# Kernel optimization log

Measured on AMD Instinct MI355X. Metric: run time of the kernel, lower is better.

Reference implementation:

```python
import jax, jax.numpy as jnp
import numpy as np

# Video-DiT scale: d_model = H * D = 2048
B, S_T, S_C, H, D = 2, 2048, 1024, 16, 128


def setup_inputs() -> dict:
    key = jax.random.key(0)
    ks = jax.random.split(key, 6)
    f = lambda k, s: jax.random.normal(k, s, dtype=jnp.float32)
    return {
        "target_q": f(ks[0], (B, S_T, H, D)),
        "target_k": f(ks[1], (B, S_T, H, D)),
        "target_v": f(ks[2], (B, S_T, H, D)),
        "cond_k": f(ks[3], (B, S_C, H, D)),
        "cond_v": f(ks[4], (B, S_C, H, D)),
        "b_param": f(ks[5], (1,)),
    }


def reference(target_q, target_k, target_v, cond_k, cond_v, b_param):
    """Extended target self-attention over [target_k; cond_k] with a scalar
    logit bias b_param added only to the condition-key columns.
    Inputs BSHD; returns [B, S_t, H*D] (ready for output_proj)."""
    Bq, St, Hh, Dd = target_q.shape
    Sc = cond_k.shape[1]
    scale = Dd ** -0.5  # softmax_scale defaults to head_dim**-0.5

    k_ext = jnp.concatenate([target_k, cond_k], axis=1)  # [B, S_t+S_c, H, D]
    v_ext = jnp.concatenate([target_v, cond_v], axis=1)

    # [B, H, S_t, S_t+S_c]
    logits = jnp.einsum('bqhd,bkhd->bhqk', target_q, k_ext) * jnp.asarray(scale, target_q.dtype)
    # bias: 0 on target keys, b on cond keys
    bias = jnp.concatenate([
        jnp.zeros((St,), logits.dtype),
        jnp.broadcast_to(b_param.astype(logits.dtype), (Sc,)),
    ])
    logits = logits + bias[None, None, None, :]

    probs = jax.nn.softmax(logits, axis=-1)
    out = jnp.einsum('bhqk,bkhd->bqhd', probs, v_ext)  # [B, S_t, H, D]
    return out.reshape(Bq, St, Hh * Dd)
```

## Files before the change

kernel.cpp:

```cpp
#include <hip/hip_runtime.h>
#include <hip/hip_bf16.h>

typedef __attribute__((ext_vector_type(4))) float f32x4;
typedef __attribute__((ext_vector_type(16))) float f32x16;
typedef __attribute__((ext_vector_type(8))) short bf8;
typedef __attribute__((ext_vector_type(2))) int i32x2;

#define B_ 2
#define ST 2048
#define SC 1024
#define SK 3072
#define NH 16
#define DH 128
#define KVB 32
#define NT 96
#define TGT 64
#define SCALE 0.088388347648318447f
#define LOG2E 1.4426950408889634f
#define PRE_TILE_U32 2048
#define PRE_BYTES (32ull * 96 * 512 * 16)
#define WS_NEED (2ull * PRE_BYTES)

__device__ __forceinline__ i32x2 tr_read(unsigned a) {
    i32x2 d;
    asm volatile("ds_read_b64_tr_b16 %0, %1" : "=v"(d) : "v"(a));
    return d;
}

__device__ __forceinline__ unsigned cvtpk(float lo, float hi) {
    unsigned r;
    asm("v_cvt_pk_bf16_f32 %0, %1, %2" : "=v"(r) : "v"(lo), "v"(hi));
    return r;
}

__device__ __forceinline__ void swap32(unsigned &a, unsigned &b) {
    asm volatile("v_permlane32_swap_b32 %0, %1" : "+v"(a), "+v"(b));
}

__device__ __forceinline__ bf8 mk_bf8(i32x2 a, i32x2 b) {
    union { i32x2 h[2]; bf8 v; } u;
    u.h[0] = a; u.h[1] = b;
    return u.v;
}
__device__ __forceinline__ bf8 mk_bf8w(unsigned w0, unsigned w1, unsigned w2, unsigned w3) {
    union { unsigned w[4]; bf8 v; } u;
    u.w[0] = w0; u.w[1] = w1; u.w[2] = w2; u.w[3] = w3;
    return u.v;
}
__device__ __forceinline__ bf8 pack_bf8(f32x4 a, f32x4 b) {
    return mk_bf8w(cvtpk(a[0], a[1]), cvtpk(a[2], a[3]),
                   cvtpk(b[0], b[1]), cvtpk(b[2], b[3]));
}

__global__ __launch_bounds__(256)
void preconv(const float* __restrict__ TK, const float* __restrict__ TV,
             const float* __restrict__ CK, const float* __restrict__ CV,
             unsigned* __restrict__ KP, unsigned* __restrict__ VP)
{
    const unsigned gid = blockIdx.x * 256 + threadIdx.x;
    const int c    = gid & 511;
    const int idx  = gid >> 9;
    const int bhid = idx / 96;
    const int t    = idx - bhid * 96;
    const int bb   = bhid >> 4;
    const int hh   = bhid & 15;

    const int krow = c >> 4;
    const int kcol = ((c & 15) ^ (krow & 7)) << 3;
    const int gkv  = t * 32 + krow;
    const float* kp = (gkv < ST)
        ? TK + (((size_t)bb * ST + gkv) * NH + hh) * DH + kcol
        : CK + (((size_t)bb * SC + (gkv - ST)) * NH + hh) * DH + kcol;
    const f32x4 k0 = *(const f32x4*)kp;
    const f32x4 k1 = *(const f32x4*)(kp + 4);
    unsigned* ko = KP + (size_t)gid * 4;
    ko[0] = cvtpk(k0[0], k0[1]); ko[1] = cvtpk(k0[2], k0[3]);
    ko[2] = cvtpk(k1[0], k1[1]); ko[3] = cvtpk(k1[2], k1[3]);

    const int vkv = (((c >> 8) & 1) << 4) | (((c >> 4) & 1) << 3)
                  | (((c >> 7) & 1) << 2) | ((c >> 1) & 3);
    const int vd  = (((c >> 5) & 3) << 5) | (((c >> 3) & 1) << 4)
                  | ((c & 1) << 3);
    const int gvv = t * 32 + vkv;
    const float* vp = (gvv < ST)
        ? TV + (((size_t)bb * ST + gvv) * NH + hh) * DH + vd
        : CV + (((size_t)bb * SC + (gvv - ST)) * NH + hh) * DH + vd;
    const f32x4 v0 = *(const f32x4*)vp;
    const f32x4 v1 = *(const f32x4*)(vp + 4);
    unsigned* vo = VP + (size_t)gid * 4;
    vo[0] = cvtpk(v0[0], v0[1]); vo[1] = cvtpk(v0[2], v0[3]);
    vo[2] = cvtpk(v1[0], v1[1]); vo[3] = cvtpk(v1[2], v1[3]);
}

__global__ __launch_bounds__(256, 2)
void attn_fwd_pre(const float* __restrict__ Q,
                  const unsigned* __restrict__ KP,
                  const unsigned* __restrict__ VP,
                  const float* __restrict__ BP,
                  float* __restrict__ OUT)
{
    __shared__ __align__(16) unsigned short Ks[3][KVB * DH];
    __shared__ __align__(16) unsigned short Vs[3][KVB * DH];

    const int tid = threadIdx.x;
    const int w   = tid >> 6;
    const int l   = tid & 63;
    const int r31 = l & 31;
    const int hi  = l >> 5;

    const int bid = blockIdx.x;
    const int xcd = bid & 7;
    const int sub = bid >> 3;
    const int bh  = xcd * 4 + (sub >> 4);
    const int qt  = sub & 15;
    const int bb  = bh >> 4;
    const int hh  = bh & 15;
    const int bh96 = bh * 96;

    const float biasl = BP[0] * LOG2E;

    const int qrow = qt * 128 + w * 32 + r31;
    const float* qp = Q + (((size_t)bb * ST + qrow) * NH + hh) * DH;
    const float qsc = SCALE * LOG2E;
    bf8 qf[8];
#pragma unroll
    for (int dk = 0; dk < 8; ++dk) {
        const f32x4 x0 = *(const f32x4*)(qp + dk * 16 + hi * 8);
        const f32x4 x1 = *(const f32x4*)(qp + dk * 16 + hi * 8 + 4);
        qf[dk] = mk_bf8w(cvtpk(x0[0]*qsc, x0[1]*qsc), cvtpk(x0[2]*qsc, x0[3]*qsc),
                         cvtpk(x1[0]*qsc, x1[1]*qsc), cvtpk(x1[2]*qsc, x1[3]*qsc));
    }

    f32x16 oa[4];
#pragma unroll
    for (int dt = 0; dt < 4; ++dt)
#pragma unroll
        for (int e = 0; e < 16; ++e) oa[dt][e] = 0.f;
    float l_run = 0.f;

    auto stage = [&](int t, int buf) {
        const unsigned* kt = KP + (size_t)(bh96 + t) * PRE_TILE_U32;
        const unsigned* vt = VP + (size_t)(bh96 + t) * PRE_TILE_U32;
#pragma unroll
        for (int i = 0; i < 2; ++i) {
            const int cb = (w << 6) + (i << 8);
            const unsigned kdst = (unsigned)(size_t)&Ks[buf][cb * 8];
            const unsigned vdst = (unsigned)(size_t)&Vs[buf][cb * 8];
            const unsigned* kg = kt + (size_t)(cb + l) * 4;
            const unsigned* vg = vt + (size_t)(cb + l) * 4;
            __builtin_amdgcn_global_load_lds(
                (const __attribute__((address_space(1))) unsigned*)(size_t)kg,
                (__attribute__((address_space(3))) unsigned*)(size_t)kdst, 16, 0, 0);
            __builtin_amdgcn_global_load_lds(
                (const __attribute__((address_space(1))) unsigned*)(size_t)vg,
                (__attribute__((address_space(3))) unsigned*)(size_t)vdst, 16, 0, 0);
        }
    };

    stage(0, 0);
    stage(1, 1);

    const unsigned vLane = (unsigned)(size_t)&Vs[0][0]
                         + (unsigned)((l >> 4) * 128 + (l & 15) * 8);

    int buf = 0;
    for (int t = 0; t < NT; ++t) {
        if (t < NT - 1) asm volatile("s_waitcnt vmcnt(4)" ::: "memory");
        else            asm volatile("s_waitcnt vmcnt(0)" ::: "memory");
        __builtin_amdgcn_s_barrier();
        asm volatile("" ::: "memory");
        if (t + 2 < NT) {
            const int nb = (buf + 2 >= 3) ? buf - 1 : buf + 2;
            stage(t + 2, nb);
        }
        const float bias = (t >= TGT) ? biasl : 0.f;
        const char* kB = (const char*)Ks[0] + (unsigned)buf * 8192u;

        f32x16 s0;
#pragma unroll
        for (int e = 0; e < 16; ++e) s0[e] = bias;
        __builtin_amdgcn_s_setprio(1);
#pragma unroll
        for (int dk = 0; dk < 8; ++dk) {
            int o = r31 * 256 + (dk * 16 + hi * 8) * 2;
            o ^= (r31 & 7) << 4;
            const bf8 kf = *(const bf8*)(kB + o);
            s0 = __builtin_amdgcn_mfma_f32_32x32x16_bf16(kf, qf[dk], s0, 0, 0, 0);
        }
        __builtin_amdgcn_s_setprio(0);

        asm volatile("" ::: "memory");
        const unsigned vA = vLane + (unsigned)buf * 8192u;
        i32x2 vt_[2][4][2];
#pragma unroll
        for (int ks = 0; ks < 2; ++ks) {
            const unsigned vk = vA + (unsigned)(ks << 12);
#pragma unroll
            for (int dt = 0; dt < 4; ++dt) {
                vt_[ks][dt][0] = tr_read(vk + dt * 512);
                vt_[ks][dt][1] = tr_read(vk + dt * 512 + 2048);
            }
        }

        float rs = 0.f;
#pragma unroll
        for (int e = 0; e < 16; ++e) {
            s0[e] = __builtin_amdgcn_exp2f(s0[e]);
            rs += s0[e];
        }
        l_run += rs;

        unsigned a0 = cvtpk(s0[0], s0[1]),  b0 = cvtpk(s0[4], s0[5]);
        unsigned a1 = cvtpk(s0[2], s0[3]),  b1 = cvtpk(s0[6], s0[7]);
        swap32(a0, b0); swap32(a1, b1);
        const bf8 pf0 = mk_bf8w(a0, a1, b0, b1);
        unsigned a2 = cvtpk(s0[8], s0[9]),   b2 = cvtpk(s0[12], s0[13]);
        unsigned a3 = cvtpk(s0[10], s0[11]), b3 = cvtpk(s0[14], s0[15]);
        swap32(a2, b2); swap32(a3, b3);
        const bf8 pf1 = mk_bf8w(a2, a3, b2, b3);

        asm volatile("s_waitcnt lgkmcnt(0)");
        __builtin_amdgcn_sched_barrier(0);
        __builtin_amdgcn_s_setprio(1);
#pragma unroll
        for (int ks = 0; ks < 2; ++ks) {
            const bf8 pf = ks ? pf1 : pf0;
#pragma unroll
            for (int dt = 0; dt < 4; ++dt) {
                const bf8 vf = mk_bf8(vt_[ks][dt][0], vt_[ks][dt][1]);
                oa[dt] = __builtin_amdgcn_mfma_f32_32x32x16_bf16(vf, pf, oa[dt], 0, 0, 0);
            }
        }
        __builtin_amdgcn_s_setprio(0);

        buf = (buf == 2) ? 0 : buf + 1;
    }

    const float l_tot = l_run + __shfl_xor(l_run, 32);
    const float inv = 1.0f / l_tot;
    float* op = OUT + ((size_t)(bb * ST + qrow)) * (NH * DH) + hh * DH;
#pragma unroll
    for (int dt = 0; dt < 4; ++dt)
#pragma unroll
        for (int rr = 0; rr < 4; ++rr) {
            f32x4 st;
            st[0] = oa[dt][rr * 4 + 0] * inv;
            st[1] = oa[dt][rr * 4 + 1] * inv;
            st[2] = oa[dt][rr * 4 + 2] * inv;
            st[3] = oa[dt][rr * 4 + 3] * inv;
            *(f32x4*)(op + dt * 32 + rr * 8 + hi * 4) = st;
        }
}

__global__ __launch_bounds__(256, 2)
void attn_fwd_reg(const float* __restrict__ Q,
                  const float* __restrict__ TK,
                  const float* __restrict__ TV,
                  const float* __restrict__ CK,
                  const float* __restrict__ CV,
                  const float* __restrict__ BP,
                  float* __restrict__ OUT)
{
    __shared__ __align__(16) unsigned short Ks[2][KVB * DH];
    __shared__ __align__(16) unsigned short Vs[2][KVB * DH];

    const int tid = threadIdx.x;
    const int w   = tid >> 6;
    const int l   = tid & 63;
    const int r31 = l & 31;
    const int hi  = l >> 5;

    const int bid = blockIdx.x;
    const int xcd = bid & 7;
    const int sub = bid >> 3;
    const int bh  = xcd * 4 + (sub >> 4);
    const int qt  = sub & 15;
    const int bb  = bh >> 4;
    const int hh  = bh & 15;

    const float biasl = BP[0] * LOG2E;

    const int qrow = qt * 128 + w * 32 + r31;
    const float* qp = Q + (((size_t)bb * ST + qrow) * NH + hh) * DH;
    const float qsc = SCALE * LOG2E;
    bf8 qf[8];
#pragma unroll
    for (int dk = 0; dk < 8; ++dk) {
        const f32x4 x0 = *(const f32x4*)(qp + dk * 16 + hi * 8);
        const f32x4 x1 = *(const f32x4*)(qp + dk * 16 + hi * 8 + 4);
        qf[dk] = mk_bf8w(cvtpk(x0[0]*qsc, x0[1]*qsc), cvtpk(x0[2]*qsc, x0[3]*qsc),
                         cvtpk(x1[0]*qsc, x1[1]*qsc), cvtpk(x1[2]*qsc, x1[3]*qsc));
    }

    f32x16 oa[4];
#pragma unroll
    for (int dt = 0; dt < 4; ++dt)
#pragma unroll
        for (int e = 0; e < 16; ++e) oa[dt][e] = 0.f;
    float l_run = 0.f;

    f32x4 skr[2][2], svr[2][2];

    auto stage_load = [&](int t) {
        const int kv0 = t * KVB;
        const float *kb, *vb;
        if (kv0 < ST) {
            const size_t off = (((size_t)bb * ST + kv0) * NH + hh) * DH;
            kb = TK + off; vb = TV + off;
        } else {
            const size_t off = (((size_t)bb * SC + (kv0 - ST)) * NH + hh) * DH;
            kb = CK + off; vb = CV + off;
        }
#pragma unroll
        for (int i = 0; i < 2; ++i) {
            const int c = tid + (i << 8);
            const int krow = c >> 4;
            const int kcol = ((c & 15) ^ (krow & 7)) << 3;
            const float* kp = kb + (size_t)krow * (NH * DH) + kcol;
            skr[i][0] = *(const f32x4*)kp;
            skr[i][1] = *(const f32x4*)(kp + 4);
            const int vkv = (((c >> 8) & 1) << 4) | (((c >> 4) & 1) << 3)
                          | (((c >> 7) & 1) << 2) | ((c >> 1) & 3);
            const int vd  = (((c >> 5) & 3) << 5) | (((c >> 3) & 1) << 4)
                          | ((c & 1) << 3);
            const float* vp = vb + (size_t)vkv * (NH * DH) + vd;
            svr[i][0] = *(const f32x4*)vp;
            svr[i][1] = *(const f32x4*)(vp + 4);
        }
    };
    auto stage_write = [&](int buf) {
#pragma unroll
        for (int i = 0; i < 2; ++i) {
            const int c = tid + (i << 8);
            *(bf8*)((char*)Ks[buf] + c * 16) = pack_bf8(skr[i][0], skr[i][1]);
            *(bf8*)((char*)Vs[buf] + c * 16) = pack_bf8(svr[i][0], svr[i][1]);
        }
    };

    stage_load(0);
    stage_write(0);

    const unsigned vLane = (unsigned)(size_t)&Vs[0][0]
                         + (unsigned)((l >> 4) * 128 + (l & 15) * 8);

    for (int t = 0; t < NT; ++t) {
        __syncthreads();
        if (t + 1 < NT) stage_load(t + 1);
        const int buf = t & 1;
        const float bias = (t >= TGT) ? biasl : 0.f;

        f32x16 s0;
#pragma unroll
        for (int e = 0; e < 16; ++e) s0[e] = bias;
        __builtin_amdgcn_s_setprio(1);
#pragma unroll
        for (int dk = 0; dk < 8; ++dk) {
            int o = r31 * 256 + (dk * 16 + hi * 8) * 2;
            o ^= (r31 & 7) << 4;
            const bf8 kf = *(const bf8*)((const char*)Ks[buf] + o);
            s0 = __builtin_amdgcn_mfma_f32_32x32x16_bf16(kf, qf[dk], s0, 0, 0, 0);
        }
        __builtin_amdgcn_s_setprio(0);

        asm volatile("" ::: "memory");
        const unsigned vA = vLane + (unsigned)(buf << 13);
        i32x2 vt_[2][4][2];
#pragma unroll
        for (int ks = 0; ks < 2; ++ks) {
            const unsigned vk = vA + (unsigned)(ks << 12);
#pragma unroll
            for (int dt = 0; dt < 4; ++dt) {
                vt_[ks][dt][0] = tr_read(vk + dt * 512);
                vt_[ks][dt][1] = tr_read(vk + dt * 512 + 2048);
            }
        }

        if (t + 1 < NT) stage_write(buf ^ 1);

        float rs = 0.f;
#pragma unroll
        for (int e = 0; e < 16; ++e) {
            s0[e] = __builtin_amdgcn_exp2f(s0[e]);
            rs += s0[e];
        }
        l_run += rs;

        unsigned a0 = cvtpk(s0[0], s0[1]),  b0 = cvtpk(s0[4], s0[5]);
        unsigned a1 = cvtpk(s0[2], s0[3]),  b1 = cvtpk(s0[6], s0[7]);
        swap32(a0, b0); swap32(a1, b1);
        const bf8 pf0 = mk_bf8w(a0, a1, b0, b1);
        unsigned a2 = cvtpk(s0[8], s0[9]),   b2 = cvtpk(s0[12], s0[13]);
        unsigned a3 = cvtpk(s0[10], s0[11]), b3 = cvtpk(s0[14], s0[15]);
        swap32(a2, b2); swap32(a3, b3);
        const bf8 pf1 = mk_bf8w(a2, a3, b2, b3);

        asm volatile("s_waitcnt lgkmcnt(0)");
        __builtin_amdgcn_sched_barrier(0);
        __builtin_amdgcn_s_setprio(1);
#pragma unroll
        for (int ks = 0; ks < 2; ++ks) {
            const bf8 pf = ks ? pf1 : pf0;
#pragma unroll
            for (int dt = 0; dt < 4; ++dt) {
                const bf8 vf = mk_bf8(vt_[ks][dt][0], vt_[ks][dt][1]);
                oa[dt] = __builtin_amdgcn_mfma_f32_32x32x16_bf16(vf, pf, oa[dt], 0, 0, 0);
            }
        }
        __builtin_amdgcn_s_setprio(0);
    }

    const float l_tot = l_run + __shfl_xor(l_run, 32);
    const float inv = 1.0f / l_tot;
    float* op = OUT + ((size_t)(bb * ST + qrow)) * (NH * DH) + hh * DH;
#pragma unroll
    for (int dt = 0; dt < 4; ++dt)
#pragma unroll
        for (int rr = 0; rr < 4; ++rr) {
            f32x4 st;
            st[0] = oa[dt][rr * 4 + 0] * inv;
            st[1] = oa[dt][rr * 4 + 1] * inv;
            st[2] = oa[dt][rr * 4 + 2] * inv;
            st[3] = oa[dt][rr * 4 + 3] * inv;
            *(f32x4*)(op + dt * 32 + rr * 8 + hi * 4) = st;
        }
}

extern "C" void kernel_launch(void* const* d_in, const int* in_sizes, int n_in,
                              void* d_out, int out_size, void* d_ws, size_t ws_size,
                              hipStream_t stream) {
    const float* q  = (const float*)d_in[0];
    const float* tk = (const float*)d_in[1];
    const float* tv = (const float*)d_in[2];
    const float* ck = (const float*)d_in[3];
    const float* cv = (const float*)d_in[4];
    const float* bp = (const float*)d_in[5];
    float* out = (float*)d_out;

    if (ws_size >= WS_NEED) {
        unsigned* kp = (unsigned*)d_ws;
        unsigned* vp = (unsigned*)((char*)d_ws + PRE_BYTES);
        preconv<<<dim3(6144), 256, 0, stream>>>(tk, tv, ck, cv, kp, vp);
        attn_fwd_pre<<<dim3(512), 256, 0, stream>>>(q, kp, vp, bp, out);
    } else {
        attn_fwd_reg<<<dim3(512), 256, 0, stream>>>(q, tk, tv, ck, cv, bp, out);
    }
}
```

Baseline: 141.6 us.

## Software-pipeline QK of the next KV tile ahead of the current tile's softmax and PV

The main loop is restructured so the QK^T MFMAs for tile t+1 are issued before the exp/convert and PV MFMAs of tile t. Two ping-pong score accumulators are used and the loop is unrolled by two. V transpose reads are split into two halves so the second half's LDS reads overlap the first half's PV MFMAs. The launch-bounds hint becomes an explicit waves_per_eu(2,2). This aims to hide softmax latency behind matrix work. In exchange it adds 16 live accumulator registers and a stricter vmcnt(0) wait on every iteration.

Result: no change. 142.4 us (+0.6%).

```diff
diff --git a/kernel.cpp b/kernel.cpp
--- a/kernel.cpp
+++ b/kernel.cpp
@@ -92,7 +92,7 @@
     vo[2] = cvtpk(v1[0], v1[1]); vo[3] = cvtpk(v1[2], v1[3]);
 }
 
-__global__ __launch_bounds__(256, 2)
+__global__ __launch_bounds__(256) __attribute__((amdgpu_waves_per_eu(2, 2)))
 void attn_fwd_pre(const float* __restrict__ Q,
                   const unsigned* __restrict__ KP,
                   const unsigned* __restrict__ VP,
@@ -157,83 +157,101 @@
         }
     };
 
-    stage(0, 0);
-    stage(1, 1);
-
     const unsigned vLane = (unsigned)(size_t)&Vs[0][0]
                          + (unsigned)((l >> 4) * 128 + (l & 15) * 8);
-
-    int buf = 0;
-    for (int t = 0; t < NT; ++t) {
-        if (t < NT - 1) asm volatile("s_waitcnt vmcnt(4)" ::: "memory");
-        else            asm volatile("s_waitcnt vmcnt(0)" ::: "memory");
-        __builtin_amdgcn_s_barrier();
-        asm volatile("" ::: "memory");
-        if (t + 2 < NT) {
-            const int nb = (buf + 2 >= 3) ? buf - 1 : buf + 2;
-            stage(t + 2, nb);
-        }
-        const float bias = (t >= TGT) ? biasl : 0.f;
-        const char* kB = (const char*)Ks[0] + (unsigned)buf * 8192u;
-
-        f32x16 s0;
-#pragma unroll
-        for (int e = 0; e < 16; ++e) s0[e] = bias;
+    const char* kBase = (const char*)Ks[0];
+
+    auto qk_into = [&](f32x16& SN, int bufn, float biasn) {
+#pragma unroll
+        for (int e = 0; e < 16; ++e) SN[e] = biasn;
+        const char* kB = kBase + (unsigned)bufn * 8192u;
         __builtin_amdgcn_s_setprio(1);
 #pragma unroll
         for (int dk = 0; dk < 8; ++dk) {
             int o = r31 * 256 + (dk * 16 + hi * 8) * 2;
             o ^= (r31 & 7) << 4;
             const bf8 kf = *(const bf8*)(kB + o);
-            s0 = __builtin_amdgcn_mfma_f32_32x32x16_bf16(kf, qf[dk], s0, 0, 0, 0);
+            SN = __builtin_amdgcn_mfma_f32_32x32x16_bf16(kf, qf[dk], SN, 0, 0, 0);
         }
         __builtin_amdgcn_s_setprio(0);
-
+    };
+
+    stage(0, 0);
+    stage(1, 1);
+    asm volatile("s_waitcnt vmcnt(4)" ::: "memory");
+    __builtin_amdgcn_s_barrier();
+    asm volatile("" ::: "memory");
+    f32x16 sA, sB;
+    qk_into(sA, 0, 0.f);
+
+    int b0 = 0, b1 = 1, b2 = 2;
+
+    auto body = [&](int t, f32x16& SCr, f32x16& SNr) {
+        if (t + 1 < NT) asm volatile("s_waitcnt vmcnt(0)" ::: "memory");
+        __builtin_amdgcn_s_barrier();
         asm volatile("" ::: "memory");
-        const unsigned vA = vLane + (unsigned)buf * 8192u;
-        i32x2 vt_[2][4][2];
-#pragma unroll
-        for (int ks = 0; ks < 2; ++ks) {
-            const unsigned vk = vA + (unsigned)(ks << 12);
-#pragma unroll
-            for (int dt = 0; dt < 4; ++dt) {
-                vt_[ks][dt][0] = tr_read(vk + dt * 512);
-                vt_[ks][dt][1] = tr_read(vk + dt * 512 + 2048);
-            }
+        if (t + 2 < NT) stage(t + 2, b2);
+
+        if (t + 1 < NT)
+            qk_into(SNr, b1, (t + 1 >= TGT) ? biasl : 0.f);
+
+        const unsigned vA = vLane + (unsigned)b0 * 8192u;
+        i32x2 t0_[4][2];
+#pragma unroll
+        for (int dt = 0; dt < 4; ++dt) {
+            t0_[dt][0] = tr_read(vA + dt * 512);
+            t0_[dt][1] = tr_read(vA + dt * 512 + 2048);
         }
 
         float rs = 0.f;
 #pragma unroll
         for (int e = 0; e < 16; ++e) {
-            s0[e] = __builtin_amdgcn_exp2f(s0[e]);
-            rs += s0[e];
+            SCr[e] = __builtin_amdgcn_exp2f(SCr[e]);
+            rs += SCr[e];
         }
         l_run += rs;
 
-        unsigned a0 = cvtpk(s0[0], s0[1]),  b0 = cvtpk(s0[4], s0[5]);
-        unsigned a1 = cvtpk(s0[2], s0[3]),  b1 = cvtpk(s0[6], s0[7]);
-        swap32(a0, b0); swap32(a1, b1);
-        const bf8 pf0 = mk_bf8w(a0, a1, b0, b1);
-        unsigned a2 = cvtpk(s0[8], s0[9]),   b2 = cvtpk(s0[12], s0[13]);
-        unsigned a3 = cvtpk(s0[10], s0[11]), b3 = cvtpk(s0[14], s0[15]);
-        swap32(a2, b2); swap32(a3, b3);
-        const bf8 pf1 = mk_bf8w(a2, a3, b2, b3);
-
+        unsigned a0 = cvtpk(SCr[0], SCr[1]),  c0 = cvtpk(SCr[4], SCr[5]);
+        unsigned a1 = cvtpk(SCr[2], SCr[3]),  c1 = cvtpk(SCr[6], SCr[7]);
+        swap32(a0, c0); swap32(a1, c1);
+        const bf8 pf0 = mk_bf8w(a0, a1, c0, c1);
+        unsigned a2 = cvtpk(SCr[8], SCr[9]),   c2 = cvtpk(SCr[12], SCr[13]);
+        unsigned a3 = cvtpk(SCr[10], SCr[11]), c3 = cvtpk(SCr[14], SCr[15]);
+        swap32(a2, c2); swap32(a3, c3);
+        const bf8 pf1 = mk_bf8w(a2, a3, c2, c3);
+
+        asm volatile("s_waitcnt lgkmcnt(0)");
+        __builtin_amdgcn_sched_barrier(0);
+        i32x2 t1_[4][2];
+#pragma unroll
+        for (int dt = 0; dt < 4; ++dt) {
+            t1_[dt][0] = tr_read(vA + 4096 + dt * 512);
+            t1_[dt][1] = tr_read(vA + 4096 + dt * 512 + 2048);
+        }
+        __builtin_amdgcn_s_setprio(1);
+#pragma unroll
+        for (int dt = 0; dt < 4; ++dt) {
+            const bf8 vf = mk_bf8(t0_[dt][0], t0_[dt][1]);
+            oa[dt] = __builtin_amdgcn_mfma_f32_32x32x16_bf16(vf, pf0, oa[dt], 0, 0, 0);
+        }
+        __builtin_amdgcn_s_setprio(0);
         asm volatile("s_waitcnt lgkmcnt(0)");
         __builtin_amdgcn_sched_barrier(0);
         __builtin_amdgcn_s_setprio(1);
 #pragma unroll
-        for (int ks = 0; ks < 2; ++ks) {
-            const bf8 pf = ks ? pf1 : pf0;
-#pragma unroll
-            for (int dt = 0; dt < 4; ++dt) {
-                const bf8 vf = mk_bf8(vt_[ks][dt][0], vt_[ks][dt][1]);
-                oa[dt] = __builtin_amdgcn_mfma_f32_32x32x16_bf16(vf, pf, oa[dt], 0, 0, 0);
-            }
+        for (int dt = 0; dt < 4; ++dt) {
+            const bf8 vf = mk_bf8(t1_[dt][0], t1_[dt][1]);
+            oa[dt] = __builtin_amdgcn_mfma_f32_32x32x16_bf16(vf, pf1, oa[dt], 0, 0, 0);
         }
         __builtin_amdgcn_s_setprio(0);
 
-        buf = (buf == 2) ? 0 : buf + 1;
+        const int n0 = b1, n1 = b2, n2 = b0;
+        b0 = n0; b1 = n1; b2 = n2;
+    };
+
+    for (int t = 0; t < NT; t += 2) {
+        body(t, sA, sB);
+        body(t + 1, sB, sA);
     }
 
     const float l_tot = l_run + __shfl_xor(l_run, 32);
```
